# Performance work log

Hardware: AMD Instinct MI355X
Metric: run time of the kernel (lower is better)

The kernel has to match this reference:

```python
import jax, jax.numpy as jnp
import numpy as np

N_E, N_C, N_DL, N_IT, N_EP, N_HA, N_CA, N_AS = 11964, 188, 100, 7, 100, 10, 10, 7
D = 128
B, S = 256, 400
N_V = N_E + 1      # hypergraph vertices (exercises)
N_HE = N_C + 1     # hyperedges (concepts)
MEMB = 3           # concept memberships per exercise
BN_EPS = 1e-5


def _hg_v2v_mean(X, pair_v, pair_e):
    # HGNN+ smoothing: vertex -> hyperedge (mean) -> vertex (mean)
    ones_e = jnp.ones(pair_e.shape, X.dtype)
    e_deg = jnp.clip(jax.ops.segment_sum(ones_e, pair_e, num_segments=N_HE), 1.0)
    v_deg = jnp.clip(jax.ops.segment_sum(ones_e, pair_v, num_segments=N_V), 1.0)
    E = jax.ops.segment_sum(X[pair_v], pair_e, num_segments=N_HE) / e_deg[:, None]
    return jax.ops.segment_sum(E[pair_e], pair_v, num_segments=N_V) / v_deg[:, None]


def _hgnnp_conv(X, W, b, gamma, beta, mean, var, pair_v, pair_e, is_last):
    X = X @ W + b
    X = (X - mean) * jax.lax.rsqrt(var + BN_EPS) * gamma + beta  # eval-mode BN
    X = _hg_v2v_mean(X, pair_v, pair_e)
    if not is_last:
        X = jax.nn.relu(X)
    return X


def setup_inputs() -> dict:
    key = jax.random.key(0)
    ks = jax.random.split(key, 32)
    inp = {}
    inp['input_e'] = jax.random.randint(ks[0], (B, S), 0, N_V)
    inp['input_ed'] = jax.random.randint(ks[1], (B, S), 0, N_DL + 1)
    inp['input_ep'] = jax.random.randint(ks[2], (B, S), 0, N_EP + 1)
    inp['input_a'] = jax.random.randint(ks[3], (B, S), 0, 2)
    inp['input_as'] = jax.random.randint(ks[4], (B, S), 0, N_AS + 1)
    inp['input_ha'] = jax.random.randint(ks[5], (B, S), 0, N_HA + 1)
    inp['input_ca'] = jax.random.randint(ks[6], (B, S), 0, N_CA + 1)
    inp['input_it'] = jax.random.randint(ks[7], (B, S), 0, N_IT + 1)
    inp['deliver_h'] = jnp.zeros((B, D), jnp.float32)
    # hypergraph incidence (exercise-concept Q-matrix edges)
    rng = np.random.default_rng(0)
    inp['pair_v'] = jnp.asarray(np.repeat(np.arange(N_V), MEMB))
    inp['pair_e'] = jnp.asarray(rng.integers(0, N_HE, size=N_V * MEMB))
    inp['ec_map'] = jax.random.randint(ks[8], (N_V,), 0, N_HE)
    inp['ecd_map'] = jax.random.randint(ks[9], (N_V,), 0, N_DL + 1)
    # embedding tables (xavier-ish scale)
    def emb(k, n):
        return jax.random.normal(k, (n, D), jnp.float32) * 0.05
    inp['e_table'] = emb(ks[10], N_V)
    inp['c_table'] = emb(ks[11], N_HE)
    inp['ed_table'] = emb(ks[12], N_DL + 1)
    inp['cd_table'] = emb(ks[13], N_DL + 1)
    inp['a_table'] = emb(ks[14], 2)
    inp['it_table'] = emb(ks[15], N_IT + 1)
    inp['ep_table'] = emb(ks[16], N_EP + 1)
    inp['ha_table'] = emb(ks[17], N_HA + 1)
    inp['ca_table'] = emb(ks[18], N_CA + 1)
    inp['as_table'] = emb(ks[19], N_AS + 1)
    # HGNNP conv 1 & 2
    def lin(k, din, dout):
        return jax.random.normal(k, (din, dout), jnp.float32) * (1.0 / np.sqrt(din))
    inp['W1'] = lin(ks[20], D, D); inp['b1'] = jnp.zeros((D,), jnp.float32)
    inp['g1'] = jnp.ones((D,), jnp.float32); inp['be1'] = jnp.zeros((D,), jnp.float32)
    inp['m1'] = jnp.zeros((D,), jnp.float32); inp['v1'] = jnp.ones((D,), jnp.float32)
    inp['W2'] = lin(ks[21], D, D); inp['b2'] = jnp.zeros((D,), jnp.float32)
    inp['g2'] = jnp.ones((D,), jnp.float32); inp['be2'] = jnp.zeros((D,), jnp.float32)
    inp['m2'] = jnp.zeros((D,), jnp.float32); inp['v2'] = jnp.ones((D,), jnp.float32)
    # linear_i: (d_e + d_dl + d_ep + d_c + d_dl) -> d_x
    inp['Wi'] = lin(ks[22], 5 * D, D); inp['bi'] = jnp.zeros((D,), jnp.float32)
    # GRU knowledge-state cell: input = concat(x, a_emb) -> 2D, hidden D, 3 gates
    inp['Wg'] = lin(ks[23], 2 * D, 3 * D)
    inp['Ug'] = lin(ks[24], D, 3 * D)
    inp['bg'] = jnp.zeros((3 * D,), jnp.float32)
    # linear_predicting_e: d_x -> 1
    inp['We'] = lin(ks[25], D, 1); inp['beo'] = jnp.zeros((1,), jnp.float32)
    # linear_predicting_s: 4*d -> 1
    inp['Ws'] = lin(ks[26], 4 * D, 1); inp['bs'] = jnp.zeros((1,), jnp.float32)
    return inp


def reference(input_e, input_ed, input_ep, input_a, input_as, input_ha, input_ca, input_it,
              deliver_h, pair_v, pair_e, ec_map, ecd_map,
              e_table, c_table, ed_table, cd_table, a_table, it_table, ep_table,
              ha_table, ca_table, as_table,
              W1, b1, g1, be1, m1, v1, W2, b2, g2, be2, m2, v2,
              Wi, bi, Wg, Ug, bg, We, beo, Ws, bs):
    # 2-layer HGNN+ over the exercise hypergraph
    X = _hgnnp_conv(e_table, W1, b1, g1, be1, m1, v1, pair_v, pair_e, is_last=False)
    X = _hgnnp_conv(X, W2, b2, g2, be2, m2, v2, pair_v, pair_e, is_last=True)
    # embedding gathers  [B,S,D]
    e_emb = X[input_e]
    c_emb = c_table[ec_map[input_e]]
    cd_emb = cd_table[ecd_map[input_e]]
    ed_emb = ed_table[input_ed]
    ep_emb = ep_table[input_ep]
    x = jnp.tanh(jnp.concatenate([e_emb, ed_emb, ep_emb, c_emb, cd_emb], -1) @ Wi + bi)  # [B,S,D]
    a_emb = a_table[input_a]
    xs = jnp.moveaxis(jnp.concatenate([x, a_emb], -1), 1, 0)  # [S,B,2D]
    xp = jnp.moveaxis(x, 1, 0)                                # [S,B,D]

    def step(h, inputs):
        xin, xq = inputs
        y = jax.nn.sigmoid((h * xq) @ We + beo)[..., 0]  # predict from prior knowledge state
        gi = xin @ Wg + bg
        gh = h @ Ug
        iz, ir, inn = jnp.split(gi, 3, -1)
        hz, hr, hn = jnp.split(gh, 3, -1)
        z = jax.nn.sigmoid(iz + hz)
        r = jax.nn.sigmoid(ir + hr)
        n = jnp.tanh(inn + r * hn)
        return (1.0 - z) * n + z * h, y

    _, ys = jax.lax.scan(step, deliver_h, (xs, xp))
    pred_main = jnp.moveaxis(ys, 0, 1)  # [B,S]
    s_in = jnp.concatenate([ha_table[input_ha], ca_table[input_ca],
                            as_table[input_as], it_table[input_it]], -1)
    pred_s = jax.nn.sigmoid(s_in @ Ws + bs)[..., 0]  # [B,S]
    return pred_s, pred_main
```

## Files before the change

kernel.cpp:

```cpp
#include <hip/hip_runtime.h>

#define N_V   11965
#define N_HE  189
#define NPAIR 35895
#define BB    256
#define SS    400
#define DD    128
#define BSR   102400
#define NVD   (N_V * DD)

typedef __bf16 bf16x8 __attribute__((ext_vector_type(8)));
typedef float  f32x4  __attribute__((ext_vector_type(4)));

__device__ __forceinline__ ushort f2bf(float f) {
    unsigned x = __float_as_uint(f);
    return (ushort)((x + 0x7FFFu + ((x >> 16) & 1u)) >> 16);
}
__device__ __forceinline__ float bf2f(ushort u) { return __uint_as_float(((unsigned)u) << 16); }
__device__ __forceinline__ float sigm(float x) { return 1.f / (1.f + __expf(-x)); }
__device__ __forceinline__ float tanh_f(float x) { return 2.f * sigm(2.f * x) - 1.f; }
__device__ __forceinline__ float blo(unsigned u) { return __uint_as_float(u << 16); }
__device__ __forceinline__ float bhi(unsigned u) { return __uint_as_float(u); }

struct P1Args {
    const int* pair_e;
    const float *b1, *g1, *be1, *m1, *v1;
    const float *b2, *g2, *be2, *m2, *v2;
    const float *W1, *W2, *Wi, *Wg, *Ug, *e_t;
    const float *ed_t, *ep_t, *c_t, *cd_t, *a_t, *bi, *bg;
    const float *ha_t, *ca_t, *as_t, *it_t, *Ws;
    int* e_deg;
    float* aff;
    ushort *W1T, *W2T, *WiTe, *WgT, *UgT, *e_tb;
    float *edW, *epW, *cW, *cdW, *agi, *sd;
};

__global__ __launch_bounds__(384) void p1_kernel(P1Args A) {
    int bid = blockIdx.x, t = threadIdx.x;
    if (bid == 0) {
        if (t < 128) {
            float s = A.g1[t] * rsqrtf(A.v1[t] + 1e-5f);
            A.aff[t] = s;
            A.aff[128 + t] = A.b1[t] * s + A.be1[t] - A.m1[t] * s;
        } else if (t < 256) {
            int d = t - 128;
            float s = A.g2[d] * rsqrtf(A.v2[d] + 1e-5f);
            A.aff[256 + d] = s;
            A.aff[384 + d] = A.b2[d] * s + A.be2[d] - A.m2[d] * s;
        }
        return;
    }
    bid -= 1;
    if (bid < 94) {
        int p = bid * 384 + t;
        if (p < NPAIR) atomicAdd(&A.e_deg[A.pair_e[p]], 1);
        return;
    }
    bid -= 94;
    if (bid < 43) {
        int i = bid * 384 + t;
        if (i < 16384) { int k = i >> 7, n = i & 127; A.W1T[n * 128 + k] = f2bf(A.W1[i]); }
        return;
    }
    bid -= 43;
    if (bid < 43) {
        int i = bid * 384 + t;
        if (i < 16384) { int k = i >> 7, n = i & 127; A.W2T[n * 128 + k] = f2bf(A.W2[i]); }
        return;
    }
    bid -= 43;
    if (bid < 43) {
        int i = bid * 384 + t;
        if (i < 16384) { int k = i >> 7, n = i & 127; A.WiTe[n * 128 + k] = f2bf(A.Wi[i]); }
        return;
    }
    bid -= 43;
    if (bid < 128) {
        int i = bid * 384 + t;
        if (i < 49152) { int k = i / 384, n = i % 384; A.WgT[n * 128 + k] = f2bf(A.Wg[i]); }
        return;
    }
    bid -= 128;
    if (bid < 128) {
        int i = bid * 384 + t;
        if (i < 49152) { int k = i / 384, n = i % 384; A.UgT[n * 128 + k] = f2bf(A.Ug[i]); }
        return;
    }
    bid -= 128;
    if (bid < 998) {
        int i4 = bid * 1536 + t * 4;
        if (i4 < NVD) {
            float4 v = *(const float4*)(A.e_t + i4);
            ushort4 o;
            o.x = f2bf(v.x); o.y = f2bf(v.y); o.z = f2bf(v.z); o.w = f2bf(v.w);
            *(ushort4*)(A.e_tb + i4) = o;
        }
        return;
    }
    bid -= 998;
    if (bid < 101) {
        if (t < 128) {
            float acc = 0.f;
            for (int k = 0; k < 128; ++k)
                acc += A.ed_t[bid * 128 + k] * A.Wi[(128 + k) * 128 + t];
            A.edW[bid * 128 + t] = acc + A.bi[t];
        }
        return;
    }
    bid -= 101;
    if (bid < 101) {
        if (t < 128) {
            float acc = 0.f;
            for (int k = 0; k < 128; ++k)
                acc += A.ep_t[bid * 128 + k] * A.Wi[(256 + k) * 128 + t];
            A.epW[bid * 128 + t] = acc;
        }
        return;
    }
    bid -= 101;
    if (bid < 189) {
        if (t < 128) {
            float acc = 0.f;
            for (int k = 0; k < 128; ++k)
                acc += A.c_t[bid * 128 + k] * A.Wi[(384 + k) * 128 + t];
            A.cW[bid * 128 + t] = acc;
        }
        return;
    }
    bid -= 189;
    if (bid < 101) {
        if (t < 128) {
            float acc = 0.f;
            for (int k = 0; k < 128; ++k)
                acc += A.cd_t[bid * 128 + k] * A.Wi[(512 + k) * 128 + t];
            A.cdW[bid * 128 + t] = acc;
        }
        return;
    }
    bid -= 101;
    if (bid < 2) {
        float acc = 0.f;
        for (int k = 0; k < 128; ++k)
            acc += A.a_t[bid * 128 + k] * A.Wg[(128 + k) * 384 + t];
        A.agi[bid * 384 + t] = acc + A.bg[t];
        return;
    }
    bid -= 2;
    {
        int r = bid;
        const float* tab; int woff, row;
        if (r < 11)      { tab = A.ha_t; row = r;      woff = 0;   }
        else if (r < 22) { tab = A.ca_t; row = r - 11; woff = 128; }
        else if (r < 30) { tab = A.as_t; row = r - 22; woff = 256; }
        else             { tab = A.it_t; row = r - 30; woff = 384; }
        if (t < 64) {
            float p = tab[row * 128 + t] * A.Ws[woff + t]
                    + tab[row * 128 + 64 + t] * A.Ws[woff + 64 + t];
            #pragma unroll
            for (int o = 32; o > 0; o >>= 1) p += __shfl_xor(p, o);
            if (t == 0) A.sd[r] = p;
        }
    }
}

__global__ __launch_bounds__(384) void csr_build(
    const int* __restrict__ e_deg, const int* __restrict__ pair_e,
    const int* __restrict__ pair_v, int* __restrict__ start,
    int* __restrict__ cursor, int* __restrict__ list) {
    __shared__ int sc[256];
    __shared__ int sx[256];
    int t = threadIdx.x;
    int d = 0;
    if (t < 256) { d = (t < N_HE) ? e_deg[t] : 0; sc[t] = d; }
    __syncthreads();
    for (int off = 1; off < 256; off <<= 1) {
        int v = (t < 256 && t >= off) ? sc[t - off] : 0;
        __syncthreads();
        if (t < 256) sc[t] += v;
        __syncthreads();
    }
    if (t < 256) sx[t] = sc[t] - d;
    __syncthreads();
    if (blockIdx.x == 0) {
        if (t < N_HE) start[t] = sx[t];
        if (t == 0) start[N_HE] = sc[N_HE - 1];
    }
    int p = blockIdx.x * 384 + t;
    if (p < NPAIR) {
        int e = pair_e[p];
        int pos = atomicAdd(&cursor[e], 1);
        list[sx[e] + pos] = pair_v[p];
    }
}

__global__ __launch_bounds__(256) void gemm_mfma8(
    const ushort* __restrict__ Amat, const ushort* __restrict__ BT,
    float* __restrict__ out, int M,
    const float* __restrict__ colS, const float* __restrict__ colB) {
    int lane = threadIdx.x & 63, wave = threadIdx.x >> 6;
    int q = lane >> 4, c = lane & 15;
    int rowbase = blockIdx.x * 64 + wave * 16;
    int arow = rowbase + c;
    if (arow > M - 1) arow = M - 1;
    f32x4 acc[8];
#pragma unroll
    for (int i = 0; i < 8; ++i) acc[i] = (f32x4){0.f, 0.f, 0.f, 0.f};
#pragma unroll
    for (int ko = 0; ko < 4; ++ko) {
        bf16x8 af = *(const bf16x8*)(Amat + (size_t)arow * 128 + ko * 32 + q * 8);
#pragma unroll
        for (int nt = 0; nt < 8; ++nt) {
            bf16x8 bfr = *(const bf16x8*)(BT + (size_t)(nt * 16 + c) * 128 + ko * 32 + q * 8);
            acc[nt] = __builtin_amdgcn_mfma_f32_16x16x32_bf16(af, bfr, acc[nt], 0, 0, 0);
        }
    }
#pragma unroll
    for (int nt = 0; nt < 8; ++nt) {
        int col = nt * 16 + c;
        float s = colS ? colS[col] : 1.f;
        float bb = colB ? colB[col] : 0.f;
#pragma unroll
        for (int r = 0; r < 4; ++r) {
            int row = rowbase + q * 4 + r;
            if (row < M) out[(size_t)row * 128 + col] = acc[nt][r] * s + bb;
        }
    }
}

__global__ __launch_bounds__(256) void gemm_gi(
    const ushort* __restrict__ Amat, const ushort* __restrict__ BT,
    ushort* __restrict__ out, const float* __restrict__ agi,
    const int* __restrict__ aidx,
    const int* __restrict__ ha, const int* __restrict__ ca,
    const int* __restrict__ as_, const int* __restrict__ it,
    const float* __restrict__ sd, const float* __restrict__ bs,
    float* __restrict__ outs) {
    int lane = threadIdx.x & 63, wave = threadIdx.x >> 6;
    int q = lane >> 4, c = lane & 15;
    int rowbase = blockIdx.x * 64 + wave * 16;
    int arow = rowbase + c;
    f32x4 acc[24];
#pragma unroll
    for (int i = 0; i < 24; ++i) acc[i] = (f32x4){0.f, 0.f, 0.f, 0.f};
#pragma unroll
    for (int ko = 0; ko < 4; ++ko) {
        bf16x8 af = *(const bf16x8*)(Amat + (size_t)arow * 128 + ko * 32 + q * 8);
#pragma unroll
        for (int nt = 0; nt < 24; ++nt) {
            bf16x8 bfr = *(const bf16x8*)(BT + (size_t)(nt * 16 + c) * 128 + ko * 32 + q * 8);
            acc[nt] = __builtin_amdgcn_mfma_f32_16x16x32_bf16(af, bfr, acc[nt], 0, 0, 0);
        }
    }
#pragma unroll
    for (int nt = 0; nt < 24; ++nt) {
        int col = nt * 16 + c;
#pragma unroll
        for (int r = 0; r < 4; ++r) {
            int row = rowbase + q * 4 + r;
            float v = acc[nt][r] + agi[aidx[row] * 384 + col];
            out[(size_t)row * 384 + col] = f2bf(v);
        }
    }
    if (threadIdx.x < 64) {
        int row = blockIdx.x * 64 + threadIdx.x;
        float v = sd[ha[row]] + sd[11 + ca[row]] + sd[22 + as_[row]] + sd[30 + it[row]] + bs[0];
        outs[row] = sigm(v);
    }
}

__global__ __launch_bounds__(512) void edge_mean(const float* __restrict__ Y,
                                                 const int* __restrict__ list,
                                                 const int* __restrict__ start,
                                                 float* __restrict__ E) {
    __shared__ float red[4][128];
    int e = blockIdx.x;
    int d = threadIdx.x & 127, g = threadIdx.x >> 7;
    int s0 = start[e], n = start[e + 1] - s0;
    float acc = 0.f;
    for (int i = g; i < n; i += 4) acc += Y[(size_t)list[s0 + i] * DD + d];
    red[g][d] = acc;
    __syncthreads();
    if (g == 0) {
        float v = red[0][d] + red[1][d] + red[2][d] + red[3][d];
        E[e * DD + d] = v / (float)(n > 0 ? n : 1);
    }
}

__global__ void v_mean(const float* __restrict__ E, const int* __restrict__ pair_e,
                       ushort* __restrict__ Xo, int relu) {
    int idx = blockIdx.x * 256 + threadIdx.x;
    if (idx >= NVD) return;
    int v = idx >> 7, d = idx & 127;
    float a = E[pair_e[3 * v] * DD + d] + E[pair_e[3 * v + 1] * DD + d] +
              E[pair_e[3 * v + 2] * DD + d];
    a *= (1.f / 3.f);
    if (relu) a = fmaxf(a, 0.f);
    Xo[idx] = f2bf(a);
}

__global__ void k3_kernel(const int* __restrict__ in_e, const int* __restrict__ in_ed,
                          const int* __restrict__ in_ep, const float* __restrict__ XW,
                          const float* __restrict__ cW, const float* __restrict__ cdW,
                          const float* __restrict__ edW, const float* __restrict__ epW,
                          const int* __restrict__ ec_map, const int* __restrict__ ecd_map,
                          ushort* __restrict__ xbf) {
    int idx = blockIdx.x * 256 + threadIdx.x;
    if (idx >= BSR * 32) return;
    int row = idx >> 5, dq = (idx & 31) << 2;
    int e = in_e[row];
    float4 a = *(const float4*)(XW + (size_t)e * DD + dq);
    float4 b = *(const float4*)(cW + ec_map[e] * DD + dq);
    float4 c = *(const float4*)(cdW + ecd_map[e] * DD + dq);
    float4 d = *(const float4*)(edW + in_ed[row] * DD + dq);
    float4 g = *(const float4*)(epW + in_ep[row] * DD + dq);
    ushort4 o;
    o.x = f2bf(tanh_f(a.x + b.x + c.x + d.x + g.x));
    o.y = f2bf(tanh_f(a.y + b.y + c.y + d.y + g.y));
    o.z = f2bf(tanh_f(a.z + b.z + c.z + d.z + g.z));
    o.w = f2bf(tanh_f(a.w + b.w + c.w + d.w + g.w));
    *(ushort4*)(xbf + (size_t)row * DD + dq) = o;
}

__global__ void
__attribute__((amdgpu_flat_work_group_size(768, 768)))
gru_scan(
    const ushort* __restrict__ gi, const ushort* __restrict__ xb,
    const ushort* __restrict__ UgT, const float* __restrict__ h0,
    const float* __restrict__ We, const float* __restrict__ beo_p,
    float* __restrict__ out) {
    __shared__ __align__(16) float h_s[128];
    __shared__ float p_s[128];
    __shared__ float pp[4][392];
    int b = blockIdx.x, t = threadIdx.x;
    int kq = t / 192;
    int cp = t % 192;
    const uint4* WA = (const uint4*)(UgT + (size_t)cp * 128 + kq * 32);
    const uint4* WB = (const uint4*)(UgT + (size_t)(cp + 192) * 128 + kq * 32);
    uint4 A0 = WA[0], A1 = WA[1], A2 = WA[2], A3 = WA[3];
    uint4 B0 = WB[0], B1 = WB[1], B2 = WB[2], B3 = WB[3];
    unsigned a0 = A0.x, a1 = A0.y, a2 = A0.z, a3 = A0.w;
    unsigned a4 = A1.x, a5 = A1.y, a6 = A1.z, a7 = A1.w;
    unsigned a8 = A2.x, a9 = A2.y, a10 = A2.z, a11 = A2.w;
    unsigned a12 = A3.x, a13 = A3.y, a14 = A3.z, a15 = A3.w;
    unsigned c0 = B0.x, c1 = B0.y, c2 = B0.z, c3 = B0.w;
    unsigned c4 = B1.x, c5 = B1.y, c6 = B1.z, c7 = B1.w;
    unsigned c8 = B2.x, c9 = B2.y, c10 = B2.z, c11 = B2.w;
    unsigned c12 = B3.x, c13 = B3.y, c14 = B3.z, c15 = B3.w;
    float beo = beo_p[0];
    float wev = 0.f, hreg = 0.f;
    if (t < 128) {
        wev = We[t];
        hreg = h0[b * 128 + t];
        h_s[t] = hreg;
    }
    const ushort* gip = gi + (size_t)b * SS * 384;
    const ushort* xp = xb + (size_t)b * SS * 128;
    float gz_nx = 0.f, gr_nx = 0.f, gn_nx = 0.f, xw_nx = 0.f;
    if (t < 128) {
        gz_nx = bf2f(gip[t]);
        gr_nx = bf2f(gip[128 + t]);
        gn_nx = bf2f(gip[256 + t]);
        xw_nx = bf2f(xp[t]) * wev;
    }
    float* omain = out + BSR + b * SS;
    __syncthreads();
    for (int s = 0; s < SS; ++s) {
#define PINA(X) asm volatile("" : "+a"(X));
        PINA(a0) PINA(a1) PINA(a2) PINA(a3) PINA(a4) PINA(a5) PINA(a6) PINA(a7)
        PINA(a8) PINA(a9) PINA(a10) PINA(a11) PINA(a12) PINA(a13) PINA(a14) PINA(a15)
        PINA(c0) PINA(c1) PINA(c2) PINA(c3) PINA(c4) PINA(c5) PINA(c6) PINA(c7)
        PINA(c8) PINA(c9) PINA(c10) PINA(c11) PINA(c12) PINA(c13) PINA(c14) PINA(c15)
#undef PINA
        float gz = gz_nx, gr = gr_nx, gn = gn_nx, xw = xw_nx;
        if (s + 1 < SS && t < 128) {
            const ushort* g2 = gip + (size_t)(s + 1) * 384;
            gz_nx = bf2f(g2[t]);
            gr_nx = bf2f(g2[128 + t]);
            gn_nx = bf2f(g2[256 + t]);
            xw_nx = bf2f(xp[(size_t)(s + 1) * 128 + t]) * wev;
        }
        const float4* h4 = (const float4*)h_s + kq * 8;
        float accA = 0.f, accB = 0.f;
#define FB2(HI, U0, U1, U2, U3, V0, V1, V2, V3) { \
        float4 hv0 = h4[HI], hv1 = h4[HI + 1]; \
        accA = fmaf(hv0.x, blo(U0), accA); accA = fmaf(hv0.y, bhi(U0), accA); \
        accA = fmaf(hv0.z, blo(U1), accA); accA = fmaf(hv0.w, bhi(U1), accA); \
        accA = fmaf(hv1.x, blo(U2), accA); accA = fmaf(hv1.y, bhi(U2), accA); \
        accA = fmaf(hv1.z, blo(U3), accA); accA = fmaf(hv1.w, bhi(U3), accA); \
        accB = fmaf(hv0.x, blo(V0), accB); accB = fmaf(hv0.y, bhi(V0), accB); \
        accB = fmaf(hv0.z, blo(V1), accB); accB = fmaf(hv0.w, bhi(V1), accB); \
        accB = fmaf(hv1.x, blo(V2), accB); accB = fmaf(hv1.y, bhi(V2), accB); \
        accB = fmaf(hv1.z, blo(V3), accB); accB = fmaf(hv1.w, bhi(V3), accB); }
        FB2(0, a0, a1, a2, a3, c0, c1, c2, c3)
        FB2(2, a4, a5, a6, a7, c4, c5, c6, c7)
        FB2(4, a8, a9, a10, a11, c8, c9, c10, c11)
        FB2(6, a12, a13, a14, a15, c12, c13, c14, c15)
#undef FB2
        pp[kq][cp] = accA;
        pp[kq][cp + 192] = accB;
        if (t >= 704 && s > 0) {
            int l = t - 704;
            float pv = p_s[l] + p_s[l + 64];
#pragma unroll
            for (int o = 32; o > 0; o >>= 1) pv += __shfl_xor(pv, o);
            if (l == 0) omain[s - 1] = sigm(pv + beo);
        }
        __syncthreads();
        if (t < 128) {
            float Sz = pp[0][t] + pp[1][t] + pp[2][t] + pp[3][t];
            float Sr = pp[0][128 + t] + pp[1][128 + t] + pp[2][128 + t] + pp[3][128 + t];
            float Sn = pp[0][256 + t] + pp[1][256 + t] + pp[2][256 + t] + pp[3][256 + t];
            float z = sigm(gz + Sz);
            float r = sigm(gr + Sr);
            float n = tanh_f(gn + r * Sn);
            p_s[t] = hreg * xw;
            hreg = (1.f - z) * n + z * hreg;
            h_s[t] = hreg;
        }
        __syncthreads();
    }
    if (t >= 704) {
        int l = t - 704;
        float pv = p_s[l] + p_s[l + 64];
#pragma unroll
        for (int o = 32; o > 0; o >>= 1) pv += __shfl_xor(pv, o);
        if (l == 0) omain[SS - 1] = sigm(pv + beo);
    }
}

extern "C" void kernel_launch(void* const* d_in, const int* in_sizes, int n_in,
                              void* d_out, int out_size, void* d_ws, size_t ws_size,
                              hipStream_t stream) {
    const int* in_e   = (const int*)d_in[0];
    const int* in_ed  = (const int*)d_in[1];
    const int* in_ep  = (const int*)d_in[2];
    const int* in_a   = (const int*)d_in[3];
    const int* in_as  = (const int*)d_in[4];
    const int* in_ha  = (const int*)d_in[5];
    const int* in_ca  = (const int*)d_in[6];
    const int* in_it  = (const int*)d_in[7];
    const float* deliver_h = (const float*)d_in[8];
    const int* pair_v = (const int*)d_in[9];
    const int* pair_e = (const int*)d_in[10];
    const int* ec_map = (const int*)d_in[11];
    const int* ecd_map= (const int*)d_in[12];
    const float* e_table  = (const float*)d_in[13];
    const float* c_table  = (const float*)d_in[14];
    const float* ed_table = (const float*)d_in[15];
    const float* cd_table = (const float*)d_in[16];
    const float* a_table  = (const float*)d_in[17];
    const float* it_table = (const float*)d_in[18];
    const float* ep_table = (const float*)d_in[19];
    const float* ha_table = (const float*)d_in[20];
    const float* ca_table = (const float*)d_in[21];
    const float* as_table = (const float*)d_in[22];
    const float* W1 = (const float*)d_in[23];
    const float* b1 = (const float*)d_in[24];
    const float* g1 = (const float*)d_in[25];
    const float* be1= (const float*)d_in[26];
    const float* m1 = (const float*)d_in[27];
    const float* v1 = (const float*)d_in[28];
    const float* W2 = (const float*)d_in[29];
    const float* b2 = (const float*)d_in[30];
    const float* g2 = (const float*)d_in[31];
    const float* be2= (const float*)d_in[32];
    const float* m2 = (const float*)d_in[33];
    const float* v2 = (const float*)d_in[34];
    const float* Wi = (const float*)d_in[35];
    const float* bi = (const float*)d_in[36];
    const float* Wg = (const float*)d_in[37];
    const float* Ug = (const float*)d_in[38];
    const float* bg = (const float*)d_in[39];
    const float* We = (const float*)d_in[40];
    const float* beo= (const float*)d_in[41];
    const float* Ws = (const float*)d_in[42];
    const float* bs = (const float*)d_in[43];
    float* out = (float*)d_out;
    char* ws = (char*)d_ws;

    size_t off = 0;
    auto alloc = [&](size_t bytes) { size_t o = off; off += (bytes + 255) & ~(size_t)255; return o; };
    size_t o_degcur = alloc(378 * 4);
    size_t o_start  = alloc(190 * 4);
    size_t o_list   = alloc((size_t)NPAIR * 4);
    size_t o_aff    = alloc(512 * 4);
    size_t o_W1T    = alloc(16384 * 2);
    size_t o_W2T    = alloc(16384 * 2);
    size_t o_WiTe   = alloc(16384 * 2);
    size_t o_WgT    = alloc(49152 * 2);
    size_t o_UgT    = alloc(49152 * 2);
    size_t o_edW    = alloc(101 * 128 * 4);
    size_t o_epW    = alloc(101 * 128 * 4);
    size_t o_cW     = alloc(189 * 128 * 4);
    size_t o_cdW    = alloc(101 * 128 * 4);
    size_t o_agi    = alloc(2 * 384 * 4);
    size_t o_sd     = alloc(38 * 4);
    size_t o_etb    = alloc((size_t)NVD * 2);
    size_t o_E      = alloc((size_t)N_HE * DD * 4);
    size_t o_Y      = alloc((size_t)NVD * 4);
    size_t o_X1     = alloc((size_t)NVD * 2);
    size_t o_X2     = alloc((size_t)NVD * 2);
    size_t o_XW     = alloc((size_t)NVD * 4);
    size_t o_xbf    = alloc((size_t)BSR * DD * 2);
    size_t o_gi     = alloc((size_t)BSR * 384 * 2);

    int*    e_deg  = (int*)(ws + o_degcur);
    int*    cursor = e_deg + 189;
    int*    startp = (int*)(ws + o_start);
    int*    listp  = (int*)(ws + o_list);
    float*  aff    = (float*)(ws + o_aff);
    ushort* W1T    = (ushort*)(ws + o_W1T);
    ushort* W2T    = (ushort*)(ws + o_W2T);
    ushort* WiTe   = (ushort*)(ws + o_WiTe);
    ushort* WgT    = (ushort*)(ws + o_WgT);
    ushort* UgTp   = (ushort*)(ws + o_UgT);
    float*  edW    = (float*)(ws + o_edW);
    float*  epW    = (float*)(ws + o_epW);
    float*  cW     = (float*)(ws + o_cW);
    float*  cdW    = (float*)(ws + o_cdW);
    float*  agi    = (float*)(ws + o_agi);
    float*  sd     = (float*)(ws + o_sd);
    ushort* e_tb   = (ushort*)(ws + o_etb);
    float*  E      = (float*)(ws + o_E);
    float*  Y      = (float*)(ws + o_Y);
    ushort* X1b    = (ushort*)(ws + o_X1);
    ushort* X2b    = (ushort*)(ws + o_X2);
    float*  XW     = (float*)(ws + o_XW);
    ushort* xbf    = (ushort*)(ws + o_xbf);
    ushort* gi     = (ushort*)(ws + o_gi);

    hipMemsetAsync(ws + o_degcur, 0, 378 * 4, stream);

    P1Args pa;
    pa.pair_e = pair_e;
    pa.b1 = b1; pa.g1 = g1; pa.be1 = be1; pa.m1 = m1; pa.v1 = v1;
    pa.b2 = b2; pa.g2 = g2; pa.be2 = be2; pa.m2 = m2; pa.v2 = v2;
    pa.W1 = W1; pa.W2 = W2; pa.Wi = Wi; pa.Wg = Wg; pa.Ug = Ug; pa.e_t = e_table;
    pa.ed_t = ed_table; pa.ep_t = ep_table; pa.c_t = c_table; pa.cd_t = cd_table;
    pa.a_t = a_table; pa.bi = bi; pa.bg = bg;
    pa.ha_t = ha_table; pa.ca_t = ca_table; pa.as_t = as_table; pa.it_t = it_table; pa.Ws = Ws;
    pa.e_deg = e_deg; pa.aff = aff;
    pa.W1T = W1T; pa.W2T = W2T; pa.WiTe = WiTe; pa.WgT = WgT; pa.UgT = UgTp; pa.e_tb = e_tb;
    pa.edW = edW; pa.epW = epW; pa.cW = cW; pa.cdW = cdW; pa.agi = agi; pa.sd = sd;
    p1_kernel<<<2010, 384, 0, stream>>>(pa);

    csr_build<<<94, 384, 0, stream>>>(e_deg, pair_e, pair_v, startp, cursor, listp);

    gemm_mfma8<<<(N_V + 63) / 64, 256, 0, stream>>>(e_tb, W1T, Y, N_V, aff, aff + 128);
    edge_mean<<<N_HE, 512, 0, stream>>>(Y, listp, startp, E);
    v_mean<<<(NVD + 255) / 256, 256, 0, stream>>>(E, pair_e, X1b, 1);
    gemm_mfma8<<<(N_V + 63) / 64, 256, 0, stream>>>(X1b, W2T, Y, N_V, aff + 256, aff + 384);
    edge_mean<<<N_HE, 512, 0, stream>>>(Y, listp, startp, E);
    v_mean<<<(NVD + 255) / 256, 256, 0, stream>>>(E, pair_e, X2b, 0);
    gemm_mfma8<<<(N_V + 63) / 64, 256, 0, stream>>>(X2b, WiTe, XW, N_V, nullptr, nullptr);
    k3_kernel<<<(BSR * 32 + 255) / 256, 256, 0, stream>>>(in_e, in_ed, in_ep, XW, cW, cdW, edW,
                                                          epW, ec_map, ecd_map, xbf);
    gemm_gi<<<BSR / 64, 256, 0, stream>>>(xbf, WgT, gi, agi, in_a,
                                          in_ha, in_ca, in_as, in_it, sd, bs, out);
    gru_scan<<<BB, 768, 0, stream>>>(gi, xbf, UgTp, deliver_h, We, beo, out);
}
```

Measured before the change: 912.1 us.

## Fold second layer BN and Wi projection into one weight, fuse embedding into gate GEMM

Result: faster. 876.0 us (-3.9%).

```diff
diff --git a/kernel.cpp b/kernel.cpp
--- a/kernel.cpp
+++ b/kernel.cpp
@@ -31,8 +31,8 @@
     const float *ha_t, *ca_t, *as_t, *it_t, *Ws;
     int* e_deg;
     float* aff;
-    ushort *W1T, *W2T, *WiTe, *WgT, *UgT, *e_tb;
-    float *edW, *epW, *cW, *cdW, *agi, *sd;
+    ushort *W1T, *W2ppT, *WgT, *UgT, *e_tb;
+    float *t2p, *edW, *epW, *cW, *cdW, *agi, *sd;
 };
 
 __global__ __launch_bounds__(384) void p1_kernel(P1Args A) {
@@ -42,11 +42,6 @@
             float s = A.g1[t] * rsqrtf(A.v1[t] + 1e-5f);
             A.aff[t] = s;
             A.aff[128 + t] = A.b1[t] * s + A.be1[t] - A.m1[t] * s;
-        } else if (t < 256) {
-            int d = t - 128;
-            float s = A.g2[d] * rsqrtf(A.v2[d] + 1e-5f);
-            A.aff[256 + d] = s;
-            A.aff[384 + d] = A.b2[d] * s + A.be2[d] - A.m2[d] * s;
         }
         return;
     }
@@ -63,18 +58,32 @@
         return;
     }
     bid -= 43;
-    if (bid < 43) {
-        int i = bid * 384 + t;
-        if (i < 16384) { int k = i >> 7, n = i & 127; A.W2T[n * 128 + k] = f2bf(A.W2[i]); }
-        return;
-    }
-    bid -= 43;
-    if (bid < 43) {
-        int i = bid * 384 + t;
-        if (i < 16384) { int k = i >> 7, n = i & 127; A.WiTe[n * 128 + k] = f2bf(A.Wi[i]); }
-        return;
-    }
-    bid -= 43;
+    if (bid < 128) {
+        int k = bid;
+        if (t < 128) {
+            float acc = 0.f;
+            for (int j = 0; j < 128; ++j) {
+                float s2 = A.g2[j] * rsqrtf(A.v2[j] + 1e-5f);
+                acc += A.W2[k * 128 + j] * s2 * A.Wi[j * 128 + t];
+            }
+            A.W2ppT[t * 128 + k] = f2bf(acc);
+        }
+        return;
+    }
+    bid -= 128;
+    if (bid < 1) {
+        if (t < 128) {
+            float acc = 0.f;
+            for (int j = 0; j < 128; ++j) {
+                float s2 = A.g2[j] * rsqrtf(A.v2[j] + 1e-5f);
+                float t2 = A.b2[j] * s2 + A.be2[j] - A.m2[j] * s2;
+                acc += t2 * A.Wi[j * 128 + t];
+            }
+            A.t2p[t] = acc;
+        }
+        return;
+    }
+    bid -= 1;
     if (bid < 128) {
         int i = bid * 384 + t;
         if (i < 49152) { int k = i / 384, n = i % 384; A.WgT[n * 128 + k] = f2bf(A.Wg[i]); }
@@ -227,24 +236,61 @@
     }
 }
 
-__global__ __launch_bounds__(256) void gemm_gi(
-    const ushort* __restrict__ Amat, const ushort* __restrict__ BT,
-    ushort* __restrict__ out, const float* __restrict__ agi,
-    const int* __restrict__ aidx,
+__global__ __launch_bounds__(256) void gemm_gi_fused(
+    const int* __restrict__ in_e, const int* __restrict__ in_ed,
+    const int* __restrict__ in_ep, const float* __restrict__ XW,
+    const float* __restrict__ cW, const float* __restrict__ cdW,
+    const float* __restrict__ edW, const float* __restrict__ epW,
+    const int* __restrict__ ec_map, const int* __restrict__ ecd_map,
+    ushort* __restrict__ xbf,
+    const ushort* __restrict__ BT, ushort* __restrict__ outg,
+    const float* __restrict__ agi, const int* __restrict__ aidx,
     const int* __restrict__ ha, const int* __restrict__ ca,
     const int* __restrict__ as_, const int* __restrict__ it,
     const float* __restrict__ sd, const float* __restrict__ bs,
     float* __restrict__ outs) {
-    int lane = threadIdx.x & 63, wave = threadIdx.x >> 6;
+    __shared__ ushort x_s[64 * 136];
+    __shared__ int se[64], sed[64], sep[64], sec[64], secd[64], sa[64];
+    int tid = threadIdx.x;
+    int rowbase_blk = blockIdx.x * 64;
+    if (tid < 64) {
+        int e = in_e[rowbase_blk + tid];
+        se[tid] = e;
+        sed[tid] = in_ed[rowbase_blk + tid];
+        sep[tid] = in_ep[rowbase_blk + tid];
+        sec[tid] = ec_map[e];
+        secd[tid] = ecd_map[e];
+        sa[tid] = aidx[rowbase_blk + tid];
+    }
+    __syncthreads();
+#pragma unroll
+    for (int i = 0; i < 8; ++i) {
+        int gidx = tid + i * 256;
+        int rl = gidx >> 5, dq = (gidx & 31) << 2;
+        int e = se[rl];
+        float4 a = *(const float4*)(XW + (size_t)e * DD + dq);
+        float4 b = *(const float4*)(cW + sec[rl] * DD + dq);
+        float4 c = *(const float4*)(cdW + secd[rl] * DD + dq);
+        float4 d = *(const float4*)(edW + sed[rl] * DD + dq);
+        float4 g = *(const float4*)(epW + sep[rl] * DD + dq);
+        ushort4 o;
+        o.x = f2bf(tanh_f(a.x + b.x + c.x + d.x + g.x));
+        o.y = f2bf(tanh_f(a.y + b.y + c.y + d.y + g.y));
+        o.z = f2bf(tanh_f(a.z + b.z + c.z + d.z + g.z));
+        o.w = f2bf(tanh_f(a.w + b.w + c.w + d.w + g.w));
+        *(ushort4*)(x_s + rl * 136 + dq) = o;
+        *(ushort4*)(xbf + (size_t)(rowbase_blk + rl) * DD + dq) = o;
+    }
+    __syncthreads();
+    int lane = tid & 63, wave = tid >> 6;
     int q = lane >> 4, c = lane & 15;
-    int rowbase = blockIdx.x * 64 + wave * 16;
-    int arow = rowbase + c;
+    int rl0 = wave * 16 + c;
     f32x4 acc[24];
 #pragma unroll
     for (int i = 0; i < 24; ++i) acc[i] = (f32x4){0.f, 0.f, 0.f, 0.f};
 #pragma unroll
     for (int ko = 0; ko < 4; ++ko) {
-        bf16x8 af = *(const bf16x8*)(Amat + (size_t)arow * 128 + ko * 32 + q * 8);
+        bf16x8 af = *(const bf16x8*)(x_s + rl0 * 136 + ko * 32 + q * 8);
 #pragma unroll
         for (int nt = 0; nt < 24; ++nt) {
             bf16x8 bfr = *(const bf16x8*)(BT + (size_t)(nt * 16 + c) * 128 + ko * 32 + q * 8);
@@ -256,13 +302,13 @@
         int col = nt * 16 + c;
 #pragma unroll
         for (int r = 0; r < 4; ++r) {
-            int row = rowbase + q * 4 + r;
-            float v = acc[nt][r] + agi[aidx[row] * 384 + col];
-            out[(size_t)row * 384 + col] = f2bf(v);
-        }
-    }
-    if (threadIdx.x < 64) {
-        int row = blockIdx.x * 64 + threadIdx.x;
+            int rl = wave * 16 + q * 4 + r;
+            float v = acc[nt][r] + agi[sa[rl] * 384 + col];
+            outg[(size_t)(rowbase_blk + rl) * 384 + col] = f2bf(v);
+        }
+    }
+    if (tid < 64) {
+        int row = rowbase_blk + tid;
         float v = sd[ha[row]] + sd[11 + ca[row]] + sd[22 + as_[row]] + sd[30 + it[row]] + bs[0];
         outs[row] = sigm(v);
     }
@@ -286,39 +332,25 @@
     }
 }
 
-__global__ void v_mean(const float* __restrict__ E, const int* __restrict__ pair_e,
-                       ushort* __restrict__ Xo, int relu) {
+__global__ void v_mean_bf(const float* __restrict__ E, const int* __restrict__ pair_e,
+                          ushort* __restrict__ Xo) {
     int idx = blockIdx.x * 256 + threadIdx.x;
     if (idx >= NVD) return;
     int v = idx >> 7, d = idx & 127;
     float a = E[pair_e[3 * v] * DD + d] + E[pair_e[3 * v + 1] * DD + d] +
               E[pair_e[3 * v + 2] * DD + d];
     a *= (1.f / 3.f);
-    if (relu) a = fmaxf(a, 0.f);
-    Xo[idx] = f2bf(a);
-}
-
-__global__ void k3_kernel(const int* __restrict__ in_e, const int* __restrict__ in_ed,
-                          const int* __restrict__ in_ep, const float* __restrict__ XW,
-                          const float* __restrict__ cW, const float* __restrict__ cdW,
-                          const float* __restrict__ edW, const float* __restrict__ epW,
-                          const int* __restrict__ ec_map, const int* __restrict__ ecd_map,
-                          ushort* __restrict__ xbf) {
+    Xo[idx] = f2bf(fmaxf(a, 0.f));
+}
+
+__global__ void v_mean_f32(const float* __restrict__ E, const int* __restrict__ pair_e,
+                           float* __restrict__ Xo) {
     int idx = blockIdx.x * 256 + threadIdx.x;
-    if (idx >= BSR * 32) return;
-    int row = idx >> 5, dq = (idx & 31) << 2;
-    int e = in_e[row];
-    float4 a = *(const float4*)(XW + (size_t)e * DD + dq);
-    float4 b = *(const float4*)(cW + ec_map[e] * DD + dq);
-    float4 c = *(const float4*)(cdW + ecd_map[e] * DD + dq);
-    float4 d = *(const float4*)(edW + in_ed[row] * DD + dq);
-    float4 g = *(const float4*)(epW + in_ep[row] * DD + dq);
-    ushort4 o;
-    o.x = f2bf(tanh_f(a.x + b.x + c.x + d.x + g.x));
-    o.y = f2bf(tanh_f(a.y + b.y + c.y + d.y + g.y));
-    o.z = f2bf(tanh_f(a.z + b.z + c.z + d.z + g.z));
-    o.w = f2bf(tanh_f(a.w + b.w + c.w + d.w + g.w));
-    *(ushort4*)(xbf + (size_t)row * DD + dq) = o;
+    if (idx >= NVD) return;
+    int v = idx >> 7, d = idx & 127;
+    float a = E[pair_e[3 * v] * DD + d] + E[pair_e[3 * v + 1] * DD + d] +
+              E[pair_e[3 * v + 2] * DD + d];
+    Xo[idx] = a * (1.f / 3.f);
 }
 
 __global__ void
@@ -483,10 +515,10 @@
     size_t o_degcur = alloc(378 * 4);
     size_t o_start  = alloc(190 * 4);
     size_t o_list   = alloc((size_t)NPAIR * 4);
-    size_t o_aff    = alloc(512 * 4);
+    size_t o_aff    = alloc(256 * 4);
     size_t o_W1T    = alloc(16384 * 2);
-    size_t o_W2T    = alloc(16384 * 2);
-    size_t o_WiTe   = alloc(16384 * 2);
+    size_t o_W2pp   = alloc(16384 * 2);
+    size_t o_t2p    = alloc(128 * 4);
     size_t o_WgT    = alloc(49152 * 2);
     size_t o_UgT    = alloc(49152 * 2);
     size_t o_edW    = alloc(101 * 128 * 4);
@@ -499,7 +531,6 @@
     size_t o_E      = alloc((size_t)N_HE * DD * 4);
     size_t o_Y      = alloc((size_t)NVD * 4);
     size_t o_X1     = alloc((size_t)NVD * 2);
-    size_t o_X2     = alloc((size_t)NVD * 2);
     size_t o_XW     = alloc((size_t)NVD * 4);
     size_t o_xbf    = alloc((size_t)BSR * DD * 2);
     size_t o_gi     = alloc((size_t)BSR * 384 * 2);
@@ -510,8 +541,8 @@
     int*    listp  = (int*)(ws + o_list);
     float*  aff    = (float*)(ws + o_aff);
     ushort* W1T    = (ushort*)(ws + o_W1T);
-    ushort* W2T    = (ushort*)(ws + o_W2T);
-    ushort* WiTe   = (ushort*)(ws + o_WiTe);
+    ushort* W2ppT  = (ushort*)(ws + o_W2pp);
+    float*  t2p    = (float*)(ws + o_t2p);
     ushort* WgT    = (ushort*)(ws + o_WgT);
     ushort* UgTp   = (ushort*)(ws + o_UgT);
     float*  edW    = (float*)(ws + o_edW);
@@ -524,7 +555,6 @@
     float*  E      = (float*)(ws + o_E);
     float*  Y      = (float*)(ws + o_Y);
     ushort* X1b    = (ushort*)(ws + o_X1);
-    ushort* X2b    = (ushort*)(ws + o_X2);
     float*  XW     = (float*)(ws + o_XW);
     ushort* xbf    = (ushort*)(ws + o_xbf);
     ushort* gi     = (ushort*)(ws + o_gi);
@@ -540,22 +570,21 @@
     pa.a_t = a_table; pa.bi = bi; pa.bg = bg;
     pa.ha_t = ha_table; pa.ca_t = ca_table; pa.as_t = as_table; pa.it_t = it_table; pa.Ws = Ws;
     pa.e_deg = e_deg; pa.aff = aff;
-    pa.W1T = W1T; pa.W2T = W2T; pa.WiTe = WiTe; pa.WgT = WgT; pa.UgT = UgTp; pa.e_tb = e_tb;
-    pa.edW = edW; pa.epW = epW; pa.cW = cW; pa.cdW = cdW; pa.agi = agi; pa.sd = sd;
-    p1_kernel<<<2010, 384, 0, stream>>>(pa);
+    pa.W1T = W1T; pa.W2ppT = W2ppT; pa.WgT = WgT; pa.UgT = UgTp; pa.e_tb = e_tb;
+    pa.t2p = t2p; pa.edW = edW; pa.epW = epW; pa.cW = cW; pa.cdW = cdW;
+    pa.agi = agi; pa.sd = sd;
+    p1_kernel<<<2053, 384, 0, stream>>>(pa);
 
     csr_build<<<94, 384, 0, stream>>>(e_deg, pair_e, pair_v, startp, cursor, listp);
 
     gemm_mfma8<<<(N_V + 63) / 64, 256, 0, stream>>>(e_tb, W1T, Y, N_V, aff, aff + 128);
     edge_mean<<<N_HE, 512, 0, stream>>>(Y, listp, startp, E);
-    v_mean<<<(NVD + 255) / 256, 256, 0, stream>>>(E, pair_e, X1b, 1);
-    gemm_mfma8<<<(N_V + 63) / 64, 256, 0, stream>>>(X1b, W2T, Y, N_V, aff + 256, aff + 384);
+    v_mean_bf<<<(NVD + 255) / 256, 256, 0, stream>>>(E, pair_e, X1b);
+    gemm_mfma8<<<(N_V + 63) / 64, 256, 0, stream>>>(X1b, W2ppT, Y, N_V, nullptr, t2p);
     edge_mean<<<N_HE, 512, 0, stream>>>(Y, listp, startp, E);
-    v_mean<<<(NVD + 255) / 256, 256, 0, stream>>>(E, pair_e, X2b, 0);
-    gemm_mfma8<<<(N_V + 63) / 64, 256, 0, stream>>>(X2b, WiTe, XW, N_V, nullptr, nullptr);
-    k3_kernel<<<(BSR * 32 + 255) / 256, 256, 0, stream>>>(in_e, in_ed, in_ep, XW, cW, cdW, edW,
-                                                          epW, ec_map, ecd_map, xbf);
-    gemm_gi<<<BSR / 64, 256, 0, stream>>>(xbf, WgT, gi, agi, in_a,
-                                          in_ha, in_ca, in_as, in_it, sd, bs, out);
+    v_mean_f32<<<(NVD + 255) / 256, 256, 0, stream>>>(E, pair_e, XW);
+    gemm_gi_fused<<<BSR / 64, 256, 0, stream>>>(in_e, in_ed, in_ep, XW, cW, cdW, edW, epW,
+                                                ec_map, ecd_map, xbf, WgT, gi, agi, in_a,
+                                                in_ha, in_ca, in_as, in_it, sd, bs, out);
     gru_scan<<<BB, 768, 0, stream>>>(gi, xbf, UgTp, deliver_h, We, beo, out);
 }
```
